# Kernel tuning notes

Measured on AMD Instinct MI355X. Metric: run time of the kernel, lower is better.

Reference implementation:

```python
import jax, jax.numpy as jnp
import numpy as np

B, S, D = 8, 1024, 1024
H, HD = 16, 64  # multiheads, head_dim; H*HD == D


def setup_inputs() -> dict:
    key = jax.random.key(0)
    ks = jax.random.split(key, 6)
    mk = lambda k, shape, scale=1.0: (jax.random.normal(k, shape, dtype=jnp.float32) * scale)
    return {
        "Q_seq": mk(ks[0], (B, S, D)),
        "K_seq": mk(ks[1], (B, S, D)),
        "V_seq": mk(ks[2], (B, S, D)),
        # nn.Linear weights stored as (out_features, in_features)
        "WQ": mk(ks[3], (H * HD, D), scale=D ** -0.5),
        "WK": mk(ks[4], (H * HD, D), scale=D ** -0.5),
        "WV": mk(ks[5], (H * HD, D), scale=D ** -0.5),
    }


def _attn(Q_seq, K_seq, V_seq, WQ, WK, WV):
    # projections (Linear: x @ W.T), then split heads -> [B, H, S, HD]
    def proj(x, W):
        y = jnp.einsum('bsd,od->bso', x, W)
        return y.reshape(x.shape[0], -1, H, HD).transpose(0, 2, 1, 3)
    Q, K, V = proj(Q_seq, WQ), proj(K_seq, WK), proj(V_seq, WV)
    scale = 1.0 / jnp.sqrt(jnp.float32(HD))
    scores = jnp.einsum('bhqd,bhkd->bhqk', Q, K) * scale  # [B,H,S,S]
    attn = jax.nn.softmax(scores, axis=-1)
    # dropout p=0.1 is identity in eval mode
    out = jnp.einsum('bhqk,bhkd->bhqd', attn, V)
    return out.transpose(0, 2, 1, 3).reshape(out.shape[0], -1, H * HD)


def reference(Q_seq, K_seq, V_seq, WQ, WK, WV):
    return _attn(Q_seq, K_seq, V_seq, WQ, WK, WV)
```

## Files before the change

kernel.cpp:

```cpp
#include <hip/hip_runtime.h>
#include <stdint.h>


#define B_N 8
#define S_N 1024
#define D_N 1024
#define H_N 16
#define HD_N 64
#define M_N (B_N * S_N)

typedef __bf16 bfrag __attribute__((ext_vector_type(8)));
typedef float f32x4 __attribute__((ext_vector_type(4)));
typedef float f32x16 __attribute__((ext_vector_type(16)));
typedef unsigned int u32;
typedef u32 u32x2 __attribute__((ext_vector_type(2)));
typedef u32 u32x4 __attribute__((ext_vector_type(4)));
typedef unsigned short u16;

__device__ __forceinline__ u16 f2bf(float f) {
  uint32_t u = __float_as_uint(f);
  u += 0x7FFFu + ((u >> 16) & 1u);
  return (u16)(u >> 16);
}

__device__ __forceinline__ void gl_lds16(const void* g, void* l) {
  __builtin_amdgcn_global_load_lds(
      (const __attribute__((address_space(1))) uint32_t*)g,
      (__attribute__((address_space(3))) uint32_t*)l, 16, 0, 0);
}

__device__ __forceinline__ u32 cvtpk(float lo, float hi) {
  u32 r;
  asm("v_cvt_pk_bf16_f32 %0, %1, %2" : "=v"(r) : "v"(lo), "v"(hi));
  return r;
}

__device__ __forceinline__ float exp2r(float x) {
#if __has_builtin(__builtin_amdgcn_exp2f)
  return __builtin_amdgcn_exp2f(x);
#else
  float r;
  asm("v_exp_f32 %0, %1" : "=v"(r) : "v"(x));
  return r;
#endif
}

__device__ __forceinline__ u32x2 pl32swap(u32 a, u32 b) {
#if __has_builtin(__builtin_amdgcn_permlane32_swap)
  return __builtin_amdgcn_permlane32_swap(a, b, false, false);
#else
  u32 sa = (u32)__shfl_xor((int)a, 32, 64), sb = (u32)__shfl_xor((int)b, 32, 64);
  const bool hi = (threadIdx.x & 32) != 0;
  u32x2 r;
  r[0] = hi ? sb : a;
  r[1] = hi ? b : sa;
  return r;
#endif
}

__device__ __forceinline__ float xhalf_max(float v) {
  u32x2 r = pl32swap(__float_as_uint(v), __float_as_uint(v));
  return fmaxf(__uint_as_float(r[0]), __uint_as_float(r[1]));
}
__device__ __forceinline__ float xhalf_add(float v) {
  u32x2 r = pl32swap(__float_as_uint(v), __float_as_uint(v));
  return __uint_as_float(r[0]) + __uint_as_float(r[1]);
}

__global__ __launch_bounds__(512, 1) void gemm_qkv(
    const float* __restrict__ Qs, const float* __restrict__ Ks,
    const float* __restrict__ Vs, const float* __restrict__ WQ,
    const float* __restrict__ WK, const float* __restrict__ WV,
    u16* __restrict__ Ybf) {
  const int bid = blockIdx.x;
  const int wid = (bid & 7) * 96 + (bid >> 3);
  const int mat = wid >> 8;
  const int rem = wid & 255;
  const int m0 = (rem >> 3) * 256;
  const int n0 = (rem & 7) * 128;

  const float* A = mat == 0 ? Qs : (mat == 1 ? Ks : Vs);
  const float* Bw = mat == 0 ? WQ : (mat == 1 ? WK : WV);
  u16* Y = Ybf + (size_t)mat * (M_N * D_N);

  __shared__ u16 Ast[2][4][4096];
  __shared__ u16 Bst[2][2][4096];

  const int t = threadIdx.x;
  const int w = t >> 6, l = t & 63;
  const int lr = l & 15, lg = l >> 4;
  const int wm = w >> 1, wn = w & 1;

  const float* aSrc = A + (size_t)(m0 + (t >> 3)) * D_N + (t & 7) * 8;
  const float* bSrc = Bw + (size_t)(n0 + (t >> 3)) * D_N + (t & 7) * 8;
  const int dst8 = (t >> 3) * 64 + ((((t & 7) ^ ((t >> 3) & 7))) << 3);

  const int asw = (lr & 7) << 3;
  const int koff0 = (lg * 8) ^ asw;
  const int koff1 = (32 + lg * 8) ^ asw;

  float4 ra[4][2], rw[2][2];

#define LOADT(tt)                                                             \
  do {                                                                        \
    _Pragma("unroll") for (int c_ = 0; c_ < 4; ++c_) {                        \
      ra[c_][0] = *(const float4*)(aSrc + (size_t)(c_ * 64) * D_N + (tt)*64); \
      ra[c_][1] =                                                             \
          *(const float4*)(aSrc + (size_t)(c_ * 64) * D_N + (tt)*64 + 4);     \
    }                                                                         \
    _Pragma("unroll") for (int c_ = 0; c_ < 2; ++c_) {                        \
      rw[c_][0] = *(const float4*)(bSrc + (size_t)(c_ * 64) * D_N + (tt)*64); \
      rw[c_][1] =                                                             \
          *(const float4*)(bSrc + (size_t)(c_ * 64) * D_N + (tt)*64 + 4);     \
    }                                                                         \
  } while (0)
#define WRITET(buf)                                                           \
  do {                                                                        \
    _Pragma("unroll") for (int c_ = 0; c_ < 4; ++c_) {                        \
      u32x4 pk_;                                                              \
      pk_[0] = cvtpk(ra[c_][0].x, ra[c_][0].y);                               \
      pk_[1] = cvtpk(ra[c_][0].z, ra[c_][0].w);                               \
      pk_[2] = cvtpk(ra[c_][1].x, ra[c_][1].y);                               \
      pk_[3] = cvtpk(ra[c_][1].z, ra[c_][1].w);                               \
      *(u32x4*)(&Ast[buf][c_][dst8]) = pk_;                                   \
    }                                                                         \
    _Pragma("unroll") for (int c_ = 0; c_ < 2; ++c_) {                        \
      u32x4 pk_;                                                              \
      pk_[0] = cvtpk(rw[c_][0].x, rw[c_][0].y);                               \
      pk_[1] = cvtpk(rw[c_][0].z, rw[c_][0].w);                               \
      pk_[2] = cvtpk(rw[c_][1].x, rw[c_][1].y);                               \
      pk_[3] = cvtpk(rw[c_][1].z, rw[c_][1].w);                               \
      *(u32x4*)(&Bst[buf][c_][dst8]) = pk_;                                   \
    }                                                                         \
  } while (0)
#define LDA8(AR, buf)                                                         \
  do {                                                                        \
    const u16* p_ = &Ast[buf][wm][lr * 64];                                   \
    _Pragma("unroll") for (int mf_ = 0; mf_ < 4; ++mf_) {                     \
      AR[mf_][0] = *(const bfrag*)(p_ + mf_ * 1024 + koff0);                  \
      AR[mf_][1] = *(const bfrag*)(p_ + mf_ * 1024 + koff1);                  \
    }                                                                         \
  } while (0)
#define LDB4(BR, buf, h)                                                      \
  do {                                                                        \
    const u16* p_ = &Bst[buf][wn][((h)*32 + lr) * 64];                        \
    BR[0][0] = *(const bfrag*)(p_ + koff0);                                   \
    BR[0][1] = *(const bfrag*)(p_ + koff1);                                   \
    BR[1][0] = *(const bfrag*)(p_ + 1024 + koff0);                            \
    BR[1][1] = *(const bfrag*)(p_ + 1024 + koff1);                            \
  } while (0)
#define MMAH(h, AR, BR)                                                       \
  do {                                                                        \
    __builtin_amdgcn_s_setprio(1);                                            \
    _Pragma("unroll") for (int mf_ = 0; mf_ < 4; ++mf_)                       \
    _Pragma("unroll") for (int j_ = 0; j_ < 2; ++j_)                          \
    _Pragma("unroll") for (int kk_ = 0; kk_ < 2; ++kk_)                       \
      acc[mf_][(h)*2 + j_] = __builtin_amdgcn_mfma_f32_16x16x32_bf16(         \
          AR[mf_][kk_], BR[j_][kk_], acc[mf_][(h)*2 + j_], 0, 0, 0);          \
    __builtin_amdgcn_s_setprio(0);                                            \
  } while (0)
#define BARR()                                                                \
  __builtin_amdgcn_s_barrier();                                               \
  __builtin_amdgcn_sched_barrier(0)
#define WAITL()                                                               \
  asm volatile("s_waitcnt lgkmcnt(0)" ::: "memory");                          \
  __builtin_amdgcn_sched_barrier(0)
#define WAITV0()                                                              \
  asm volatile("s_waitcnt vmcnt(0)" ::: "memory");                            \
  __builtin_amdgcn_sched_barrier(0)

  f32x4 acc[4][4];
#pragma unroll
  for (int i = 0; i < 4; ++i)
#pragma unroll
    for (int j = 0; j < 4; ++j) acc[i][j] = (f32x4){0.f, 0.f, 0.f, 0.f};

  LOADT(0);
  WAITV0();
  WRITET(0);
  LOADT(1);
  WAITL();
  BARR();

  for (int kt = 0; kt < 16; ++kt) {
    const int cb = kt & 1;
    bfrag a[4][2], b[2][2];
    LDA8(a, cb);
    LDB4(b, cb, 0);
    if (kt < 15) {
      WAITV0();
      WRITET(cb ^ 1);
      if (kt < 14) LOADT(kt + 2);
    }
    WAITL();
    MMAH(0, a, b);
    LDB4(b, cb, 1);
    WAITL();
    MMAH(1, a, b);
    BARR();
  }

  const float alpha = (mat == 0) ? 0.18033688011112042f : 1.0f;
  const int mrow = m0 + wm * 64;
  const int ncol = n0 + wn * 64;
  if (mat < 2) {
#pragma unroll
    for (int mf = 0; mf < 4; ++mf) {
      const int row0 = mrow + mf * 16 + lg * 4;
#pragma unroll
      for (int nf = 0; nf < 4; ++nf) {
        const int col = ncol + nf * 16 + lr;
#pragma unroll
        for (int r = 0; r < 4; ++r)
          Y[(size_t)(row0 + r) * D_N + col] = f2bf(acc[mf][nf][r] * alpha);
      }
    }
  } else {
    const int b = m0 >> 10;
#pragma unroll
    for (int mf = 0; mf < 4; ++mf) {
      const int s0 = (m0 & 1023) + wm * 64 + mf * 16 + lg * 4;
#pragma unroll
      for (int nf = 0; nf < 4; ++nf) {
        const int col = ncol + nf * 16 + lr;
        const f32x4 v = acc[mf][nf];
        ushort4 pk;
        pk.x = f2bf(v[0]); pk.y = f2bf(v[1]);
        pk.z = f2bf(v[2]); pk.w = f2bf(v[3]);
        *(ushort4*)(Y + (size_t)(b * D_N + col) * S_N + s0) = pk;
      }
    }
  }
#undef LOADT
#undef WRITET
#undef LDA8
#undef LDB4
#undef MMAH
#undef BARR
#undef WAITL
#undef WAITV0
}

union AttnSMem {
  struct { u16 K[3][4096]; u16 V[3][4096]; } st;
  float ol[4][32 * 34];
};

__global__ __launch_bounds__(256, 3) void attn_fwd(const u16* __restrict__ Yq,
                                                   const u16* __restrict__ Yk,
                                                   const u16* __restrict__ Yv,
                                                   float* __restrict__ out) {
  const int bid = blockIdx.x;
  const int wid = (bid & 7) * 128 + (bid >> 3);
  const int qt = wid & 7, bh = wid >> 3;
  const int b = bh >> 4, h = bh & 15;
  const int t = threadIdx.x, w = t >> 6, l = t & 63;
  const int ln = l & 31, hi = l >> 5;

  __shared__ AttnSMem sm;

  const int qbase = qt * 128 + w * 32;

  const int row0 = w * 8 + (l >> 3);
  const int srcoff = (((l & 7) ^ ((l >> 3) & 7)) << 3);
  const u16* kS0 = Yk + ((size_t)(b * S_N + row0) * D_N + h * HD_N + srcoff);
  const u16* vS0 = Yv + ((size_t)(b * D_N + h * HD_N + row0) * S_N + srcoff);

#define STAGE(buf, tt)                                                        \
  do {                                                                        \
    const u16* ka_ = kS0 + (size_t)(tt) * 64 * D_N;                           \
    const u16* va_ = vS0 + (tt) * 64;                                         \
    gl_lds16(ka_, sm.st.K[buf] + w * 512);                                    \
    gl_lds16(ka_ + (size_t)32 * D_N, sm.st.K[buf] + 2048 + w * 512);          \
    gl_lds16(va_, sm.st.V[buf] + w * 512);                                    \
    gl_lds16(va_ + (size_t)32 * S_N, sm.st.V[buf] + 2048 + w * 512);          \
  } while (0)

  bfrag qf[4];
  {
    const u16* qp = Yq + ((size_t)(b * S_N + qbase + ln) * D_N + h * HD_N + hi * 8);
#pragma unroll
    for (int c = 0; c < 4; ++c) qf[c] = *(const bfrag*)(qp + c * 16);
  }

  STAGE(0, 0);
  STAGE(1, 1);

  int kcol[4];
#pragma unroll
  for (int c = 0; c < 4; ++c)
    kcol[c] = (((c * 32 + hi * 16) ^ ((ln & 7) << 4)) >> 1);

  f32x16 o0, o1;
#pragma unroll
  for (int r = 0; r < 16; ++r) { o0[r] = 0.f; o1[r] = 0.f; }
  float m_r = -3.0e38f, l_r = 0.f;

  asm volatile("s_waitcnt vmcnt(4)" ::: "memory");
  __builtin_amdgcn_sched_barrier(0);
  __builtin_amdgcn_s_barrier();

  int rd = 0, sb = 2;
  for (int kt = 0; kt < 16; ++kt) {
    if (kt < 14) STAGE(sb, kt + 2);

    const u16* Kb = sm.st.K[rd];
    const u16* Vb = sm.st.V[rd];

    bfrag kf[8];
#pragma unroll
    for (int s2 = 0; s2 < 2; ++s2)
#pragma unroll
      for (int c = 0; c < 4; ++c)
        kf[s2 * 4 + c] = *(const bfrag*)(Kb + (s2 * 32 + ln) * 64 + kcol[c]);

    f32x16 sa, sbv;
#pragma unroll
    for (int r = 0; r < 16; ++r) { sa[r] = 0.f; sbv[r] = 0.f; }
    __builtin_amdgcn_s_setprio(1);
#pragma unroll
    for (int c = 0; c < 4; ++c) {
      sa = __builtin_amdgcn_mfma_f32_32x32x16_bf16(kf[c], qf[c], sa, 0, 0, 0);
      sbv = __builtin_amdgcn_mfma_f32_32x32x16_bf16(kf[4 + c], qf[c], sbv, 0, 0, 0);
    }
    __builtin_amdgcn_s_setprio(0);

    bfrag vf[8];
#pragma unroll
    for (int hf = 0; hf < 2; ++hf)
#pragma unroll
      for (int c = 0; c < 4; ++c)
        vf[hf * 4 + c] = *(const bfrag*)(Vb + (hf * 32 + ln) * 64 + kcol[c]);

    float t16[16];
#pragma unroll
    for (int r = 0; r < 16; ++r) t16[r] = fmaxf(sa[r], sbv[r]);
    float t8[8];
#pragma unroll
    for (int r = 0; r < 8; ++r) t8[r] = fmaxf(t16[r], t16[r + 8]);
    float t4[4];
#pragma unroll
    for (int r = 0; r < 4; ++r) t4[r] = fmaxf(t8[r], t8[r + 4]);
    float pmax = fmaxf(fmaxf(t4[0], t4[1]), fmaxf(t4[2], t4[3]));
    pmax = xhalf_max(pmax);

    if (__any(pmax > m_r + 8.f)) {
      const float mnew = fmaxf(m_r, pmax);
      const float corr = exp2r(m_r - mnew);
#pragma unroll
      for (int r = 0; r < 16; ++r) { o0[r] *= corr; o1[r] *= corr; }
      l_r *= corr;
      m_r = mnew;
    }

#pragma unroll
    for (int r = 0; r < 16; ++r) sa[r] = exp2r(sa[r] - m_r);
#pragma unroll
    for (int r = 0; r < 16; ++r) sbv[r] = exp2r(sbv[r] - m_r);
    float s16[16];
#pragma unroll
    for (int r = 0; r < 16; ++r) s16[r] = sa[r] + sbv[r];
    float s8[8];
#pragma unroll
    for (int r = 0; r < 8; ++r) s8[r] = s16[r] + s16[r + 8];
    float s4[4];
#pragma unroll
    for (int r = 0; r < 4; ++r) s4[r] = s8[r] + s8[r + 4];
    float rsum = (s4[0] + s4[1]) + (s4[2] + s4[3]);
    l_r += xhalf_add(rsum);

    __builtin_amdgcn_s_setprio(1);
#pragma unroll
    for (int c = 0; c < 4; ++c) {
      const int bs = (c & 1) * 8;
      float p0, p1, p2, p3, p4, p5, p6, p7;
      if (c < 2) {
        p0 = sa[bs + 0]; p1 = sa[bs + 1]; p2 = sa[bs + 2]; p3 = sa[bs + 3];
        p4 = sa[bs + 4]; p5 = sa[bs + 5]; p6 = sa[bs + 6]; p7 = sa[bs + 7];
      } else {
        p0 = sbv[bs + 0]; p1 = sbv[bs + 1]; p2 = sbv[bs + 2]; p3 = sbv[bs + 3];
        p4 = sbv[bs + 4]; p5 = sbv[bs + 5]; p6 = sbv[bs + 6]; p7 = sbv[bs + 7];
      }
      const u32 x1 = cvtpk(p0, p1), x2 = cvtpk(p2, p3);
      const u32 y1 = cvtpk(p4, p5), y2 = cvtpk(p6, p7);
      const u32x2 s1 = pl32swap(x1, y1);
      const u32x2 s2 = pl32swap(x2, y2);
      union { u32 u[4]; bfrag v; } pu;
      pu.u[0] = s1[0]; pu.u[1] = s2[0]; pu.u[2] = s1[1]; pu.u[3] = s2[1];
      o0 = __builtin_amdgcn_mfma_f32_32x32x16_bf16(vf[c], pu.v, o0, 0, 0, 0);
      o1 = __builtin_amdgcn_mfma_f32_32x32x16_bf16(vf[4 + c], pu.v, o1, 0, 0, 0);
    }
    __builtin_amdgcn_s_setprio(0);

    if (kt < 14) {
      asm volatile("s_waitcnt vmcnt(4)" ::: "memory");
    } else {
      asm volatile("s_waitcnt vmcnt(0)" ::: "memory");
    }
    __builtin_amdgcn_sched_barrier(0);
    __builtin_amdgcn_s_barrier();

    rd = (rd == 2) ? 0 : rd + 1;
    sb = (sb == 2) ? 0 : sb + 1;
  }

  const float inv = 1.f / l_r;
  float* ow = sm.ol[w];
  const int qr = l >> 1, ch = l & 1;
  const float* rp = ow + qr * 34 + ch * 16;
  float* op = out + ((size_t)(b * S_N + qbase + qr) * D_N + h * HD_N + ch * 16);

#pragma unroll
  for (int g = 0; g < 4; ++g) {
    f32x4 v;
#pragma unroll
    for (int j = 0; j < 4; ++j) v[j] = o0[g * 4 + j] * inv;
    *(f32x4*)(ow + ln * 34 + g * 8 + hi * 4) = v;
  }
  asm volatile("s_waitcnt lgkmcnt(0)" ::: "memory");
  __builtin_amdgcn_sched_barrier(0);
#pragma unroll
  for (int j = 0; j < 4; ++j)
    *(f32x4*)(op + j * 4) = *(const f32x4*)(rp + j * 4);
  asm volatile("s_waitcnt lgkmcnt(0)" ::: "memory");
  __builtin_amdgcn_sched_barrier(0);

#pragma unroll
  for (int g = 0; g < 4; ++g) {
    f32x4 v;
#pragma unroll
    for (int j = 0; j < 4; ++j) v[j] = o1[g * 4 + j] * inv;
    *(f32x4*)(ow + ln * 34 + g * 8 + hi * 4) = v;
  }
  asm volatile("s_waitcnt lgkmcnt(0)" ::: "memory");
  __builtin_amdgcn_sched_barrier(0);
#pragma unroll
  for (int j = 0; j < 4; ++j)
    *(f32x4*)(op + 32 + j * 4) = *(const f32x4*)(rp + j * 4);
#undef STAGE
}

extern "C" void kernel_launch(void* const* d_in, const int* in_sizes, int n_in,
                              void* d_out, int out_size, void* d_ws, size_t ws_size,
                              hipStream_t stream) {
  const float* Qs = (const float*)d_in[0];
  const float* Ks = (const float*)d_in[1];
  const float* Vs = (const float*)d_in[2];
  const float* WQ = (const float*)d_in[3];
  const float* WK = (const float*)d_in[4];
  const float* WV = (const float*)d_in[5];
  if (ws_size < 50331648ull) return;

  u16* Ybf = (u16*)d_ws;
  float* out = (float*)d_out;

  gemm_qkv<<<dim3(768), 512, 0, stream>>>(Qs, Ks, Vs, WQ, WK, WV, Ybf);
  attn_fwd<<<dim3(1024), 256, 0, stream>>>(Ybf, Ybf + 8388608, Ybf + 16777216, out);
}
```

Measured before the change: 142.7 us.

## Halve GEMM k-tile to 32 and raise occupancy to four blocks per CU

The QKV projection GEMM now stages K-slices of 32 instead of 64, which halves the LDS buffers (from 48KB to 24KB double-buffered) and the per-thread prefetch registers, and doubles the number of k-iterations. Launch bounds go from 1 to 4 blocks per CU so several blocks can share a CU and hide the latency of global loads and barriers. In exchange the loop runs twice as many barriers and waits per unit of work, with a new swizzle pattern for 32-wide rows.

```diff
diff --git a/kernel.cpp b/kernel.cpp
--- a/kernel.cpp
+++ b/kernel.cpp
@@ -67,7 +67,7 @@
   return __uint_as_float(r[0]) + __uint_as_float(r[1]);
 }
 
-__global__ __launch_bounds__(512, 1) void gemm_qkv(
+__global__ __launch_bounds__(512, 4) void gemm_qkv(
     const float* __restrict__ Qs, const float* __restrict__ Ks,
     const float* __restrict__ Vs, const float* __restrict__ WQ,
     const float* __restrict__ WK, const float* __restrict__ WV,
@@ -83,80 +83,72 @@
   const float* Bw = mat == 0 ? WQ : (mat == 1 ? WK : WV);
   u16* Y = Ybf + (size_t)mat * (M_N * D_N);
 
-  __shared__ u16 Ast[2][4][4096];
-  __shared__ u16 Bst[2][2][4096];
+  __shared__ u16 Ast[2][8192];
+  __shared__ u16 Bst[2][4096];
 
   const int t = threadIdx.x;
   const int w = t >> 6, l = t & 63;
   const int lr = l & 15, lg = l >> 4;
   const int wm = w >> 1, wn = w & 1;
 
-  const float* aSrc = A + (size_t)(m0 + (t >> 3)) * D_N + (t & 7) * 8;
-  const float* bSrc = Bw + (size_t)(n0 + (t >> 3)) * D_N + (t & 7) * 8;
-  const int dst8 = (t >> 3) * 64 + ((((t & 7) ^ ((t >> 3) & 7))) << 3);
-
-  const int asw = (lr & 7) << 3;
-  const int koff0 = (lg * 8) ^ asw;
-  const int koff1 = (32 + lg * 8) ^ asw;
-
-  float4 ra[4][2], rw[2][2];
+  const int arow = t >> 1, ahalf = t & 1;
+  const float* aSrc = A + (size_t)(m0 + arow) * D_N + ahalf * 16;
+  const int adst0 = arow * 32 + (((ahalf * 2) ^ (arow & 3)) << 3);
+  const int adst1 = arow * 32 + (((ahalf * 2 + 1) ^ (arow & 3)) << 3);
+  const int brow = t >> 2, bq = t & 3;
+  const float* bSrc = Bw + (size_t)(n0 + brow) * D_N + bq * 8;
+  const int bdst = brow * 32 + ((bq ^ (brow & 3)) << 3);
+
+  const int koff = ((lg ^ (lr & 3)) << 3);
+
+  float4 ra[4], rw[2];
 
 #define LOADT(tt)                                                             \
   do {                                                                        \
-    _Pragma("unroll") for (int c_ = 0; c_ < 4; ++c_) {                        \
-      ra[c_][0] = *(const float4*)(aSrc + (size_t)(c_ * 64) * D_N + (tt)*64); \
-      ra[c_][1] =                                                             \
-          *(const float4*)(aSrc + (size_t)(c_ * 64) * D_N + (tt)*64 + 4);     \
-    }                                                                         \
-    _Pragma("unroll") for (int c_ = 0; c_ < 2; ++c_) {                        \
-      rw[c_][0] = *(const float4*)(bSrc + (size_t)(c_ * 64) * D_N + (tt)*64); \
-      rw[c_][1] =                                                             \
-          *(const float4*)(bSrc + (size_t)(c_ * 64) * D_N + (tt)*64 + 4);     \
-    }                                                                         \
+    const float* pa_ = aSrc + (tt)*32;                                        \
+    ra[0] = *(const float4*)(pa_ + 0);                                        \
+    ra[1] = *(const float4*)(pa_ + 4);                                        \
+    ra[2] = *(const float4*)(pa_ + 8);                                        \
+    ra[3] = *(const float4*)(pa_ + 12);                                       \
+    const float* pb_ = bSrc + (tt)*32;                                        \
+    rw[0] = *(const float4*)(pb_ + 0);                                        \
+    rw[1] = *(const float4*)(pb_ + 4);                                        \
   } while (0)
 #define WRITET(buf)                                                           \
   do {                                                                        \
-    _Pragma("unroll") for (int c_ = 0; c_ < 4; ++c_) {                        \
-      u32x4 pk_;                                                              \
-      pk_[0] = cvtpk(ra[c_][0].x, ra[c_][0].y);                               \
-      pk_[1] = cvtpk(ra[c_][0].z, ra[c_][0].w);                               \
-      pk_[2] = cvtpk(ra[c_][1].x, ra[c_][1].y);                               \
-      pk_[3] = cvtpk(ra[c_][1].z, ra[c_][1].w);                               \
-      *(u32x4*)(&Ast[buf][c_][dst8]) = pk_;                                   \
-    }                                                                         \
-    _Pragma("unroll") for (int c_ = 0; c_ < 2; ++c_) {                        \
-      u32x4 pk_;                                                              \
-      pk_[0] = cvtpk(rw[c_][0].x, rw[c_][0].y);                               \
-      pk_[1] = cvtpk(rw[c_][0].z, rw[c_][0].w);                               \
-      pk_[2] = cvtpk(rw[c_][1].x, rw[c_][1].y);                               \
-      pk_[3] = cvtpk(rw[c_][1].z, rw[c_][1].w);                               \
-      *(u32x4*)(&Bst[buf][c_][dst8]) = pk_;                                   \
-    }                                                                         \
-  } while (0)
-#define LDA8(AR, buf)                                                         \
-  do {                                                                        \
-    const u16* p_ = &Ast[buf][wm][lr * 64];                                   \
-    _Pragma("unroll") for (int mf_ = 0; mf_ < 4; ++mf_) {                     \
-      AR[mf_][0] = *(const bfrag*)(p_ + mf_ * 1024 + koff0);                  \
-      AR[mf_][1] = *(const bfrag*)(p_ + mf_ * 1024 + koff1);                  \
-    }                                                                         \
-  } while (0)
-#define LDB4(BR, buf, h)                                                      \
-  do {                                                                        \
-    const u16* p_ = &Bst[buf][wn][((h)*32 + lr) * 64];                        \
-    BR[0][0] = *(const bfrag*)(p_ + koff0);                                   \
-    BR[0][1] = *(const bfrag*)(p_ + koff1);                                   \
-    BR[1][0] = *(const bfrag*)(p_ + 1024 + koff0);                            \
-    BR[1][1] = *(const bfrag*)(p_ + 1024 + koff1);                            \
+    u32x4 p0_, p1_;                                                           \
+    p0_[0] = cvtpk(ra[0].x, ra[0].y); p0_[1] = cvtpk(ra[0].z, ra[0].w);       \
+    p0_[2] = cvtpk(ra[1].x, ra[1].y); p0_[3] = cvtpk(ra[1].z, ra[1].w);       \
+    p1_[0] = cvtpk(ra[2].x, ra[2].y); p1_[1] = cvtpk(ra[2].z, ra[2].w);       \
+    p1_[2] = cvtpk(ra[3].x, ra[3].y); p1_[3] = cvtpk(ra[3].z, ra[3].w);       \
+    *(u32x4*)(&Ast[buf][adst0]) = p0_;                                        \
+    *(u32x4*)(&Ast[buf][adst1]) = p1_;                                        \
+    u32x4 pb_;                                                                \
+    pb_[0] = cvtpk(rw[0].x, rw[0].y); pb_[1] = cvtpk(rw[0].z, rw[0].w);       \
+    pb_[2] = cvtpk(rw[1].x, rw[1].y); pb_[3] = cvtpk(rw[1].z, rw[1].w);       \
+    *(u32x4*)(&Bst[buf][bdst]) = pb_;                                         \
+  } while (0)
+#define LDA4(AR, buf)                                                         \
+  do {                                                                        \
+    const u16* p_ = &Ast[buf][(wm * 64 + lr) * 32 + koff];                    \
+    AR[0] = *(const bfrag*)(p_ + 0 * 512);                                    \
+    AR[1] = *(const bfrag*)(p_ + 1 * 512);                                    \
+    AR[2] = *(const bfrag*)(p_ + 2 * 512);                                    \
+    AR[3] = *(const bfrag*)(p_ + 3 * 512);                                    \
+  } while (0)
+#define LDB2(BR, buf, h)                                                      \
+  do {                                                                        \
+    const u16* p_ = &Bst[buf][(wn * 64 + (h)*32 + lr) * 32 + koff];           \
+    BR[0] = *(const bfrag*)(p_ + 0 * 512);                                    \
+    BR[1] = *(const bfrag*)(p_ + 1 * 512);                                    \
   } while (0)
 #define MMAH(h, AR, BR)                                                       \
   do {                                                                        \
     __builtin_amdgcn_s_setprio(1);                                            \
     _Pragma("unroll") for (int mf_ = 0; mf_ < 4; ++mf_)                       \
     _Pragma("unroll") for (int j_ = 0; j_ < 2; ++j_)                          \
-    _Pragma("unroll") for (int kk_ = 0; kk_ < 2; ++kk_)                       \
       acc[mf_][(h)*2 + j_] = __builtin_amdgcn_mfma_f32_16x16x32_bf16(         \
-          AR[mf_][kk_], BR[j_][kk_], acc[mf_][(h)*2 + j_], 0, 0, 0);          \
+          AR[mf_], BR[j_], acc[mf_][(h)*2 + j_], 0, 0, 0);                    \
     __builtin_amdgcn_s_setprio(0);                                            \
   } while (0)
 #define BARR()                                                                \
@@ -182,19 +174,19 @@
   WAITL();
   BARR();
 
-  for (int kt = 0; kt < 16; ++kt) {
+  for (int kt = 0; kt < 32; ++kt) {
     const int cb = kt & 1;
-    bfrag a[4][2], b[2][2];
-    LDA8(a, cb);
-    LDB4(b, cb, 0);
-    if (kt < 15) {
+    bfrag a[4], b[2];
+    LDA4(a, cb);
+    LDB2(b, cb, 0);
+    if (kt < 31) {
       WAITV0();
       WRITET(cb ^ 1);
-      if (kt < 14) LOADT(kt + 2);
+      if (kt < 30) LOADT(kt + 2);
     }
     WAITL();
     MMAH(0, a, b);
-    LDB4(b, cb, 1);
+    LDB2(b, cb, 1);
     WAITL();
     MMAH(1, a, b);
     BARR();
@@ -233,8 +225,8 @@
   }
 #undef LOADT
 #undef WRITET
-#undef LDA8
-#undef LDB4
+#undef LDA4
+#undef LDB2
 #undef MMAH
 #undef BARR
 #undef WAITL
```

Measured after the change: 136.9 us. 4.1% less time.
